# Performance work log

Measured on AMD Instinct MI355X. Metric: run time of the kernel, lower is better.

Reference implementation:

```python
import jax, jax.numpy as jnp
import numpy as np


def setup_inputs() -> dict:
    key = jax.random.key(0)
    ks = jax.random.split(key, 3)
    B, H, W, C = 32, 56, 56, 512
    N = H * W
    x = jax.random.normal(ks[0], (B, N, C), dtype=jnp.float32)
    # learned params (qkv_bias=False)
    w_qkv = jax.random.normal(ks[1], (C, 3 * C), dtype=jnp.float32) * (C ** -0.5)
    w_proj = jax.random.normal(ks[2], (C, C), dtype=jnp.float32) * (C ** -0.5)
    b_proj = jnp.zeros((C,), dtype=jnp.float32)
    return {"x": x, "w_qkv": w_qkv, "w_proj": w_proj, "b_proj": b_proj,
            "H": H, "W": W}


def reference(x, w_qkv, w_proj, b_proj, H, W):
    num_heads, ws = 8, 7
    B, N, C = x.shape
    hd = C // num_heads
    scale = hd ** -0.5
    hg, wg = H // ws, W // ws
    G = hg * wg  # total groups
    S = ws * ws  # tokens per window
    # window partition: [B,N,C] -> [B,G,S,C]
    xw = x.reshape(B, hg, ws, wg, ws, C).transpose(0, 1, 3, 2, 4, 5)
    xw = xw.reshape(B, G, S, C)
    # qkv projection -> [3,B,G,heads,S,hd]
    qkv = (xw @ w_qkv).reshape(B, G, S, 3, num_heads, hd)
    qkv = qkv.transpose(3, 0, 1, 4, 2, 5)
    q, k, v = qkv[0], qkv[1], qkv[2]
    attn = jnp.einsum('bghqd,bghkd->bghqk', q, k) * scale
    attn = jax.nn.softmax(attn, axis=-1)
    out = jnp.einsum('bghqk,bghkd->bghqd', attn, v)
    # merge heads: [B,G,h,S,d] -> [B,G,S,C]
    out = out.transpose(0, 1, 3, 2, 4).reshape(B, G, S, C)
    # window merge: [B,G,S,C] -> [B,N,C]
    out = out.reshape(B, hg, wg, ws, ws, C).transpose(0, 1, 3, 2, 4, 5)
    out = out.reshape(B, N, C)
    return out @ w_proj + b_proj
```

## Files before the change

### kernel.cpp

```cpp
#include <hip/hip_runtime.h>

typedef unsigned short ushort;
typedef unsigned int uint;
typedef __bf16 bf16x8 __attribute__((ext_vector_type(8)));
typedef unsigned short u16x8 __attribute__((ext_vector_type(8)));
typedef float f32x4 __attribute__((ext_vector_type(4)));

__device__ __forceinline__ ushort f2bf(float f) {
  uint u = __builtin_bit_cast(uint, f);
  u += 0x7fffu + ((u >> 16) & 1u);
  return (ushort)(u >> 16);
}

__device__ __forceinline__ f32x4 mfma_bf16(u16x8 a, u16x8 b, f32x4 c) {
  return __builtin_amdgcn_mfma_f32_16x16x32_bf16(
      __builtin_bit_cast(bf16x8, a), __builtin_bit_cast(bf16x8, b), c, 0, 0, 0);
}

__global__ __launch_bounds__(256) void cvt_x(const float* __restrict__ X,
                                             ushort* __restrict__ Xb, int total8) {
  int stride = gridDim.x * 256;
  for (int i = blockIdx.x * 256 + threadIdx.x; i < total8; i += stride) {
    f32x4 a = ((const f32x4*)X)[2 * i];
    f32x4 b = ((const f32x4*)X)[2 * i + 1];
    u16x8 o;
#pragma unroll
    for (int j = 0; j < 4; ++j) { o[j] = f2bf(a[j]); o[j + 4] = f2bf(b[j]); }
    ((u16x8*)Xb)[i] = o;
  }
}

__global__ __launch_bounds__(256) void transpose_cvt(const float* __restrict__ W,
                                                     ushort* __restrict__ WT,
                                                     int K, int N) {
  __shared__ float t[32][33];
  const int tn0 = blockIdx.x * 32, tk0 = blockIdx.y * 32;
  const int tx = threadIdx.x & 31, ty = threadIdx.x >> 5;
#pragma unroll
  for (int i = 0; i < 4; ++i) {
    int k = tk0 + ty + i * 8;
    t[ty + i * 8][tx] = W[(size_t)k * N + tn0 + tx];
  }
  __syncthreads();
#pragma unroll
  for (int i = 0; i < 4; ++i) {
    int n = tn0 + ty + i * 8;
    WT[(size_t)n * K + tk0 + tx] = f2bf(t[tx][ty + i * 8]);
  }
}


#define GLL(g, l)                                                              \
  __builtin_amdgcn_global_load_lds(                                            \
      (const __attribute__((address_space(1))) uint*)(g),                      \
      (__attribute__((address_space(3))) uint*)(l), 16, 0, 0)
#define BAR() __builtin_amdgcn_s_barrier()
#define SCB() __builtin_amdgcn_sched_barrier(0)
#define WAITV(n) asm volatile("s_waitcnt vmcnt(" #n ")" ::: "memory")

template <int OUT>
__global__ __launch_bounds__(512, 2) void gemm8p(const ushort* __restrict__ A,
                                                 const ushort* __restrict__ BT,
                                                 void* __restrict__ Cout,
                                                 const float* __restrict__ bias,
                                                 const int ldc, const int NT,
                                                 const int CPX) {
  __shared__ __align__(16) ushort as_[2][16384];
  __shared__ __align__(16) ushort bs_[2][16384];
  const int bid = blockIdx.x;
  const int wg = (bid & 7) * CPX + (bid >> 3);
  const int mt = wg / NT, nt = wg - mt * NT;
  const int m0 = mt << 8, n0 = nt << 8;
  const int tid = threadIdx.x, lane = tid & 63, wid = tid >> 6;
  const int wm = wid >> 2, wn = wid & 3;
  const int c16 = lane & 15, q4 = lane >> 4;
  const int sw = c16 & 7;
  const int lrow = lane >> 3, lcg = (lane & 7) ^ lrow;
  const ushort* Ag = A + (size_t)(m0 + wid * 16 + lrow) * 512 + lcg * 8;
  const ushort* Bg = BT + (size_t)(n0 + wid * 16 + lrow) * 512 + lcg * 8;
  const int aro = (wm * 64 + c16) * 64;
  const int bro = (wn * 32 + c16) * 64;
  const int ag0 = (q4 ^ sw) * 8;
  const int ag1 = ((4 + q4) ^ sw) * 8;

  f32x4 acc[8][4];
#pragma unroll
  for (int m = 0; m < 8; ++m)
#pragma unroll
    for (int n = 0; n < 4; ++n) acc[m][n] = f32x4{0.f, 0.f, 0.f, 0.f};
  u16x8 af[4][2], bf0[2][2], bf1[2][2];

#define STAGE_A(half, ktg)                                                     \
  do {                                                                         \
    const ushort* g_ = Ag + (size_t)(half) * (128 * 512) + (ktg) * 64;         \
    ushort* l_ = &as_[(ktg) & 1][(half) * 8192 + wid * 1024 + lane * 8];       \
    GLL(g_, l_);                                                               \
    GLL(g_ + 8 * 512, l_ + 512);                                               \
  } while (0)
#define STAGE_B(half, ktg)                                                     \
  do {                                                                         \
    const ushort* g_ = Bg + (size_t)(half) * (128 * 512) + (ktg) * 64;         \
    ushort* l_ = &bs_[(ktg) & 1][(half) * 8192 + wid * 1024 + lane * 8];       \
    GLL(g_, l_);                                                               \
    GLL(g_ + 8 * 512, l_ + 512);                                               \
  } while (0)
#define LDA(kt, mh)                                                            \
  do {                                                                         \
    const ushort* p_ = &as_[kt][(mh)*8192 + aro];                              \
    _Pragma("unroll") for (int f_ = 0; f_ < 4; ++f_) {                         \
      af[f_][0] = *(const u16x8*)(p_ + f_ * 1024 + ag0);                       \
      af[f_][1] = *(const u16x8*)(p_ + f_ * 1024 + ag1);                       \
    }                                                                          \
  } while (0)
#define LDB(kt, nh, BF)                                                        \
  do {                                                                         \
    const ushort* p_ = &bs_[kt][(nh)*8192 + bro];                              \
    _Pragma("unroll") for (int g_ = 0; g_ < 2; ++g_) {                         \
      BF[g_][0] = *(const u16x8*)(p_ + g_ * 1024 + ag0);                       \
      BF[g_][1] = *(const u16x8*)(p_ + g_ * 1024 + ag1);                       \
    }                                                                          \
  } while (0)
#define MM(mh, nh, BF)                                                         \
  do {                                                                         \
    __builtin_amdgcn_s_setprio(1);                                             \
    _Pragma("unroll") for (int f_ = 0; f_ < 4; ++f_)                           \
        _Pragma("unroll") for (int g_ = 0; g_ < 2; ++g_) {                     \
      f32x4& a_ = acc[(mh)*4 + f_][(nh)*2 + g_];                               \
      a_ = mfma_bf16(af[f_][0], BF[g_][0], a_);                                \
      a_ = mfma_bf16(af[f_][1], BF[g_][1], a_);                                \
    }                                                                          \
    __builtin_amdgcn_s_setprio(0);                                             \
  } while (0)

  STAGE_A(0, 0); STAGE_B(1, 0); STAGE_B(0, 0);
  STAGE_A(1, 0); STAGE_A(0, 1); STAGE_B(1, 1);
  WAITV(6); BAR(); SCB();

  for (int i = 0; i < 3; ++i) {
    const int k1g = 2 * i + 1, k2g = 2 * i + 2, k3g = 2 * i + 3;
    LDA(0, 0); LDB(0, 0, bf0); STAGE_A(1, k1g);
    BAR(); MM(0, 0, bf0); WAITV(10); BAR(); SCB();
    LDB(0, 1, bf1); STAGE_B(0, k1g);
    BAR(); MM(0, 1, bf1); WAITV(8); BAR(); SCB();
    LDA(0, 1); STAGE_A(0, k2g);
    BAR(); MM(1, 1, bf1); BAR(); SCB();
    STAGE_B(1, k2g);
    BAR(); MM(1, 0, bf0); WAITV(4); BAR(); SCB();
    LDA(1, 0); LDB(1, 0, bf0); STAGE_B(0, k2g);
    BAR(); MM(0, 0, bf0); WAITV(10); BAR(); SCB();
    LDB(1, 1, bf1); STAGE_A(1, k2g);
    BAR(); MM(0, 1, bf1); WAITV(10); BAR(); SCB();
    LDA(1, 1); STAGE_A(0, k3g);
    BAR(); MM(1, 1, bf1); BAR(); SCB();
    STAGE_B(1, k3g);
    BAR(); MM(1, 0, bf0); WAITV(6); BAR(); SCB();
  }
  {
    LDA(0, 0); LDB(0, 0, bf0); STAGE_A(1, 7);
    BAR(); MM(0, 0, bf0); WAITV(10); BAR(); SCB();
    LDB(0, 1, bf1); STAGE_B(0, 7);
    BAR(); MM(0, 1, bf1); WAITV(8); BAR(); SCB();
    LDA(0, 1);
    BAR(); MM(1, 1, bf1); BAR(); SCB();
    BAR(); MM(1, 0, bf0); WAITV(0); BAR(); SCB();
    LDA(1, 0); LDB(1, 0, bf0);
    BAR(); MM(0, 0, bf0); BAR(); SCB();
    LDB(1, 1, bf1);
    BAR(); MM(0, 1, bf1); BAR(); SCB();
    LDA(1, 1);
    BAR(); MM(1, 1, bf1); BAR(); SCB();
    BAR(); MM(1, 0, bf0);
  }

  const int crow = m0 + wm * 64 + q4 * 4;
  const int ccol = n0 + wn * 32 + c16;
  if constexpr (OUT == 0) {
    ushort* C = (ushort*)Cout;
#pragma unroll
    for (int mf = 0; mf < 8; ++mf) {
      const int ro = (mf >> 2) * 128 + (mf & 3) * 16;
#pragma unroll
      for (int r = 0; r < 4; ++r) {
        ushort* cp = C + (size_t)(crow + ro + r) * ldc + ccol;
        cp[0]   = f2bf(acc[mf][0][r]);
        cp[16]  = f2bf(acc[mf][1][r]);
        cp[128] = f2bf(acc[mf][2][r]);
        cp[144] = f2bf(acc[mf][3][r]);
      }
    }
  } else {
    float* C = (float*)Cout;
    const float b0 = bias[ccol], b1 = bias[ccol + 16];
    const float b2 = bias[ccol + 128], b3 = bias[ccol + 144];
#pragma unroll
    for (int mf = 0; mf < 8; ++mf) {
      const int ro = (mf >> 2) * 128 + (mf & 3) * 16;
#pragma unroll
      for (int r = 0; r < 4; ++r) {
        float* cp = C + (size_t)(crow + ro + r) * ldc + ccol;
        cp[0]   = acc[mf][0][r] + b0;
        cp[16]  = acc[mf][1][r] + b1;
        cp[128] = acc[mf][2][r] + b2;
        cp[144] = acc[mf][3][r] + b3;
      }
    }
  }
#undef STAGE_A
#undef STAGE_B
#undef LDA
#undef LDB
#undef MM
}

__global__ __launch_bounds__(256) void attn_win(const ushort* __restrict__ qkv,
                                                ushort* __restrict__ O) {
  __shared__ __align__(16) ushort p_lds[4][4096];
  __shared__ __align__(16) ushort v_lds[4][4096];
  const int tid = threadIdx.x, lane = tid & 63, w = tid >> 6;
  const int wg = blockIdx.x * 4 + w;
  const int head = wg & 7, g = (wg >> 3) & 63, b = wg >> 9;
  const int gh = g >> 3, gw = g & 7;
  const int c16 = lane & 15, q4 = lane >> 4;
  const size_t brow = (size_t)b * 3136;
  const u16x8 Z = {0, 0, 0, 0, 0, 0, 0, 0};

  int rowq[4]; bool val[4];
#pragma unroll
  for (int i = 0; i < 4; ++i) {
    int s = i * 16 + c16;
    val[i] = (s < 49);
    int ss = val[i] ? s : 0;
    rowq[i] = (gh * 7 + ss / 7) * 56 + gw * 7 + ss % 7;
  }
  const int qc = head * 64 + q4 * 8;

  u16x8 qf[2][4], kf[2][4];
#pragma unroll
  for (int i = 0; i < 4; ++i) {
    const ushort* p = qkv + (brow + rowq[i]) * 1536 + qc;
#pragma unroll
    for (int kk = 0; kk < 2; ++kk) {
      qf[kk][i] = val[i] ? *reinterpret_cast<const u16x8*>(p + kk * 32) : Z;
      kf[kk][i] = val[i] ? *reinterpret_cast<const u16x8*>(p + 512 + kk * 32) : Z;
    }
  }

  {
    int t = lane < 49 ? lane : 0;
    const ushort* vp =
        qkv + (brow + ((gh * 7 + t / 7) * 56 + gw * 7 + t % 7)) * 1536 + 1024 + head * 64;
    u16x8 vr[8];
#pragma unroll
    for (int j = 0; j < 8; ++j)
      vr[j] = (lane < 49) ? *reinterpret_cast<const u16x8*>(vp + j * 8) : Z;
#pragma unroll
    for (int d = 0; d < 64; ++d)
      v_lds[w][(d * 64 + lane) ^ ((d & 7) << 3)] = vr[d >> 3][d & 7];
  }

  f32x4 acc[4][4];
#pragma unroll
  for (int m = 0; m < 4; ++m)
#pragma unroll
    for (int n = 0; n < 4; ++n) acc[m][n] = f32x4{0.f, 0.f, 0.f, 0.f};
#pragma unroll
  for (int kk = 0; kk < 2; ++kk)
#pragma unroll
    for (int m = 0; m < 4; ++m)
#pragma unroll
      for (int n = 0; n < 4; ++n)
        acc[m][n] = mfma_bf16(qf[kk][m], kf[kk][n], acc[m][n]);

#pragma unroll
  for (int m = 0; m < 4; ++m)
#pragma unroll
    for (int r = 0; r < 4; ++r) {
      float s0 = acc[m][0][r] * 0.125f;
      float s1 = acc[m][1][r] * 0.125f;
      float s2 = acc[m][2][r] * 0.125f;
      float s3 = (c16 == 0) ? acc[m][3][r] * 0.125f : -1e30f;
      float mx = fmaxf(fmaxf(s0, s1), fmaxf(s2, s3));
#pragma unroll
      for (int off = 1; off < 16; off <<= 1) mx = fmaxf(mx, __shfl_xor(mx, off));
      s0 = __expf(s0 - mx);
      s1 = __expf(s1 - mx);
      s2 = __expf(s2 - mx);
      s3 = (c16 == 0) ? __expf(s3 - mx) : 0.f;
      float sum = s0 + s1 + s2 + s3;
#pragma unroll
      for (int off = 1; off < 16; off <<= 1) sum += __shfl_xor(sum, off);
      float inv = 1.f / sum;
      int row = m * 16 + q4 * 4 + r;
      int rb = row * 64, sw = (row & 7) << 3;
      p_lds[w][(rb + c16) ^ sw]      = f2bf(s0 * inv);
      p_lds[w][(rb + 16 + c16) ^ sw] = f2bf(s1 * inv);
      p_lds[w][(rb + 32 + c16) ^ sw] = f2bf(s2 * inv);
      p_lds[w][(rb + 48 + c16) ^ sw] = f2bf(s3 * inv);
    }
  __syncthreads();

  f32x4 o[4][4];
#pragma unroll
  for (int m = 0; m < 4; ++m)
#pragma unroll
    for (int n = 0; n < 4; ++n) o[m][n] = f32x4{0.f, 0.f, 0.f, 0.f};
#pragma unroll
  for (int kk = 0; kk < 2; ++kk) {
    u16x8 pa[4], vb[4];
#pragma unroll
    for (int m = 0; m < 4; ++m) {
      int row = m * 16 + c16;
      pa[m] = *reinterpret_cast<const u16x8*>(
          &p_lds[w][(row * 64 + kk * 32 + q4 * 8) ^ ((row & 7) << 3)]);
    }
#pragma unroll
    for (int n = 0; n < 4; ++n) {
      int d = n * 16 + c16;
      vb[n] = *reinterpret_cast<const u16x8*>(
          &v_lds[w][(d * 64 + kk * 32 + q4 * 8) ^ ((d & 7) << 3)]);
    }
#pragma unroll
    for (int m = 0; m < 4; ++m)
#pragma unroll
      for (int n = 0; n < 4; ++n) o[m][n] = mfma_bf16(pa[m], vb[n], o[m][n]);
  }

#pragma unroll
  for (int m = 0; m < 4; ++m)
#pragma unroll
    for (int r = 0; r < 4; ++r) {
      int s = m * 16 + q4 * 4 + r;
      if (s < 49) {
        int n_tok = (gh * 7 + s / 7) * 56 + gw * 7 + s % 7;
        ushort* op = O + (brow + n_tok) * 512 + head * 64 + c16;
        op[0]  = f2bf(o[m][0][r]);
        op[16] = f2bf(o[m][1][r]);
        op[32] = f2bf(o[m][2][r]);
        op[48] = f2bf(o[m][3][r]);
      }
    }
}

extern "C" void kernel_launch(void* const* d_in, const int* in_sizes, int n_in,
                              void* d_out, int out_size, void* d_ws, size_t ws_size,
                              hipStream_t stream) {
  const float* x      = (const float*)d_in[0];
  const float* w_qkv  = (const float*)d_in[1];
  const float* w_proj = (const float*)d_in[2];
  const float* b_proj = (const float*)d_in[3];
  char* ws = (char*)d_ws;
  ushort* wqkvT  = (ushort*)ws;
  ushort* wprojT = (ushort*)(ws + 1572864);
  ushort* xb     = (ushort*)(ws + 2097152);
  ushort* qkv    = (ushort*)(ws + 104857600);
  float* out = (float*)d_out;

  transpose_cvt<<<dim3(48, 16), 256, 0, stream>>>(w_qkv, wqkvT, 512, 1536);
  transpose_cvt<<<dim3(16, 16), 256, 0, stream>>>(w_proj, wprojT, 512, 512);
  cvt_x<<<2048, 256, 0, stream>>>(x, xb, 100352 * 512 / 8);
  gemm8p<0><<<2352, 512, 0, stream>>>(xb, wqkvT, (void*)qkv, nullptr, 1536, 6, 294);
  attn_win<<<4096, 256, 0, stream>>>(qkv, xb);
  gemm8p<1><<<784, 512, 0, stream>>>(xb, wprojT, (void*)out, b_proj, 512, 2, 98);
}
```

Before: 488.5 us.

## Reorder tokens into window-major layout and rework GEMM prefetch schedule

The input conversion kernel now gathers rows into window-major order, so the QKV GEMM output and the attention kernel see each 7x7 window as 49 contiguous rows. The output projection scatters rows back to the original token order in its epilogue. This replaces scattered per-token gathers in attention with contiguous row access. The GEMM main loop's stage/wait ordering is also reshuffled, with a deeper initial prefetch and different vmcnt waits, which may change how well loads overlap with MFMA work.

```diff
diff --git a/kernel.cpp b/kernel.cpp
--- a/kernel.cpp
+++ b/kernel.cpp
@@ -17,12 +17,20 @@
       __builtin_bit_cast(bf16x8, a), __builtin_bit_cast(bf16x8, b), c, 0, 0, 0);
 }
 
-__global__ __launch_bounds__(256) void cvt_x(const float* __restrict__ X,
-                                             ushort* __restrict__ Xb, int total8) {
+__device__ __forceinline__ uint win2orig(uint wr) {
+  uint b = wr / 3136u, rem = wr % 3136u;
+  uint g = rem / 49u, s = rem % 49u;
+  return b * 3136u + ((g >> 3) * 7u + s / 7u) * 56u + (g & 7u) * 7u + s % 7u;
+}
+
+__global__ __launch_bounds__(256) void cvt_x_win(const float* __restrict__ X,
+                                                 ushort* __restrict__ Xb, int total8) {
   int stride = gridDim.x * 256;
   for (int i = blockIdx.x * 256 + threadIdx.x; i < total8; i += stride) {
-    f32x4 a = ((const f32x4*)X)[2 * i];
-    f32x4 b = ((const f32x4*)X)[2 * i + 1];
+    uint wr = (uint)i >> 6, c8 = (uint)i & 63u;
+    const float* xp = X + (size_t)win2orig(wr) * 512 + c8 * 8;
+    f32x4 a = *(const f32x4*)xp;
+    f32x4 b = *(const f32x4*)(xp + 4);
     u16x8 o;
 #pragma unroll
     for (int j = 0; j < 4; ++j) { o[j] = f2bf(a[j]); o[j + 4] = f2bf(b[j]); }
@@ -132,45 +140,43 @@
     __builtin_amdgcn_s_setprio(0);                                             \
   } while (0)
 
-  STAGE_A(0, 0); STAGE_B(1, 0); STAGE_B(0, 0);
-  STAGE_A(1, 0); STAGE_A(0, 1); STAGE_B(1, 1);
-  WAITV(6); BAR(); SCB();
+  STAGE_A(0, 0); STAGE_B(0, 0); STAGE_B(1, 0); STAGE_A(1, 0);
+  STAGE_A(0, 1); STAGE_B(0, 1); STAGE_B(1, 1);
+  WAITV(10); BAR(); SCB();
 
   for (int i = 0; i < 3; ++i) {
-    const int k1g = 2 * i + 1, k2g = 2 * i + 2, k3g = 2 * i + 3;
-    LDA(0, 0); LDB(0, 0, bf0); STAGE_A(1, k1g);
+    const int o1 = 2 * i + 1, e2 = 2 * i + 2, o3 = 2 * i + 3;
+    LDA(0, 0); LDB(0, 0, bf0); STAGE_A(1, o1);
     BAR(); MM(0, 0, bf0); WAITV(10); BAR(); SCB();
-    LDB(0, 1, bf1); STAGE_B(0, k1g);
-    BAR(); MM(0, 1, bf1); WAITV(8); BAR(); SCB();
-    LDA(0, 1); STAGE_A(0, k2g);
+    LDB(0, 1, bf1); STAGE_A(0, e2);
+    BAR(); MM(0, 1, bf1); WAITV(10); BAR(); SCB();
+    LDA(0, 1); STAGE_B(0, e2);
     BAR(); MM(1, 1, bf1); BAR(); SCB();
-    STAGE_B(1, k2g);
-    BAR(); MM(1, 0, bf0); WAITV(4); BAR(); SCB();
-    LDA(1, 0); LDB(1, 0, bf0); STAGE_B(0, k2g);
+    STAGE_B(1, e2);
+    BAR(); MM(1, 0, bf0); WAITV(10); BAR(); SCB();
+    LDA(1, 0); LDB(1, 0, bf0); STAGE_A(1, e2);
     BAR(); MM(0, 0, bf0); WAITV(10); BAR(); SCB();
-    LDB(1, 1, bf1); STAGE_A(1, k2g);
+    LDB(1, 1, bf1); STAGE_A(0, o3);
     BAR(); MM(0, 1, bf1); WAITV(10); BAR(); SCB();
-    LDA(1, 1); STAGE_A(0, k3g);
+    LDA(1, 1); STAGE_B(0, o3);
     BAR(); MM(1, 1, bf1); BAR(); SCB();
-    STAGE_B(1, k3g);
-    BAR(); MM(1, 0, bf0); WAITV(6); BAR(); SCB();
-  }
-  {
-    LDA(0, 0); LDB(0, 0, bf0); STAGE_A(1, 7);
-    BAR(); MM(0, 0, bf0); WAITV(10); BAR(); SCB();
-    LDB(0, 1, bf1); STAGE_B(0, 7);
-    BAR(); MM(0, 1, bf1); WAITV(8); BAR(); SCB();
-    LDA(0, 1);
-    BAR(); MM(1, 1, bf1); BAR(); SCB();
-    BAR(); MM(1, 0, bf0); WAITV(0); BAR(); SCB();
-    LDA(1, 0); LDB(1, 0, bf0);
-    BAR(); MM(0, 0, bf0); BAR(); SCB();
-    LDB(1, 1, bf1);
-    BAR(); MM(0, 1, bf1); BAR(); SCB();
-    LDA(1, 1);
-    BAR(); MM(1, 1, bf1); BAR(); SCB();
-    BAR(); MM(1, 0, bf0);
-  }
+    STAGE_B(1, o3);
+    BAR(); MM(1, 0, bf0); WAITV(10); BAR(); SCB();
+  }
+  LDA(0, 0); LDB(0, 0, bf0); STAGE_A(1, 7);
+  BAR(); MM(0, 0, bf0); WAITV(10); BAR(); SCB();
+  LDB(0, 1, bf1);
+  BAR(); MM(0, 1, bf1); WAITV(8); BAR(); SCB();
+  LDA(0, 1);
+  BAR(); MM(1, 1, bf1); BAR(); SCB();
+  BAR(); MM(1, 0, bf0); WAITV(4); BAR(); SCB();
+  LDA(1, 0); LDB(1, 0, bf0);
+  BAR(); MM(0, 0, bf0); WAITV(2); BAR(); SCB();
+  LDB(1, 1, bf1);
+  BAR(); MM(0, 1, bf1); WAITV(0); BAR(); SCB();
+  LDA(1, 1);
+  BAR(); MM(1, 1, bf1); BAR(); SCB();
+  BAR(); MM(1, 0, bf0);
 
   const int crow = m0 + wm * 64 + q4 * 4;
   const int ccol = n0 + wn * 32 + c16;
@@ -197,7 +203,7 @@
       const int ro = (mf >> 2) * 128 + (mf & 3) * 16;
 #pragma unroll
       for (int r = 0; r < 4; ++r) {
-        float* cp = C + (size_t)(crow + ro + r) * ldc + ccol;
+        float* cp = C + (size_t)win2orig((uint)(crow + ro + r)) * 512 + ccol;
         cp[0]   = acc[mf][0][r] + b0;
         cp[16]  = acc[mf][1][r] + b1;
         cp[128] = acc[mf][2][r] + b2;
@@ -219,36 +225,26 @@
   const int tid = threadIdx.x, lane = tid & 63, w = tid >> 6;
   const int wg = blockIdx.x * 4 + w;
   const int head = wg & 7, g = (wg >> 3) & 63, b = wg >> 9;
-  const int gh = g >> 3, gw = g & 7;
   const int c16 = lane & 15, q4 = lane >> 4;
-  const size_t brow = (size_t)b * 3136;
+  const size_t wrow = (size_t)b * 3136 + g * 49;
   const u16x8 Z = {0, 0, 0, 0, 0, 0, 0, 0};
 
-  int rowq[4]; bool val[4];
+  const int qc = head * 64 + q4 * 8;
+  u16x8 qf[2][4], kf[2][4];
 #pragma unroll
   for (int i = 0; i < 4; ++i) {
     int s = i * 16 + c16;
-    val[i] = (s < 49);
-    int ss = val[i] ? s : 0;
-    rowq[i] = (gh * 7 + ss / 7) * 56 + gw * 7 + ss % 7;
-  }
-  const int qc = head * 64 + q4 * 8;
-
-  u16x8 qf[2][4], kf[2][4];
-#pragma unroll
-  for (int i = 0; i < 4; ++i) {
-    const ushort* p = qkv + (brow + rowq[i]) * 1536 + qc;
+    bool val = (s < 49);
+    const ushort* p = qkv + (wrow + (val ? s : 0)) * 1536 + qc;
 #pragma unroll
     for (int kk = 0; kk < 2; ++kk) {
-      qf[kk][i] = val[i] ? *reinterpret_cast<const u16x8*>(p + kk * 32) : Z;
-      kf[kk][i] = val[i] ? *reinterpret_cast<const u16x8*>(p + 512 + kk * 32) : Z;
+      qf[kk][i] = val ? *reinterpret_cast<const u16x8*>(p + kk * 32) : Z;
+      kf[kk][i] = val ? *reinterpret_cast<const u16x8*>(p + 512 + kk * 32) : Z;
     }
   }
 
   {
-    int t = lane < 49 ? lane : 0;
-    const ushort* vp =
-        qkv + (brow + ((gh * 7 + t / 7) * 56 + gw * 7 + t % 7)) * 1536 + 1024 + head * 64;
+    const ushort* vp = qkv + (wrow + (lane < 49 ? lane : 0)) * 1536 + 1024 + head * 64;
     u16x8 vr[8];
 #pragma unroll
     for (int j = 0; j < 8; ++j)
@@ -291,11 +287,11 @@
       for (int off = 1; off < 16; off <<= 1) sum += __shfl_xor(sum, off);
       float inv = 1.f / sum;
       int row = m * 16 + q4 * 4 + r;
-      int rb = row * 64, sw = (row & 7) << 3;
-      p_lds[w][(rb + c16) ^ sw]      = f2bf(s0 * inv);
-      p_lds[w][(rb + 16 + c16) ^ sw] = f2bf(s1 * inv);
-      p_lds[w][(rb + 32 + c16) ^ sw] = f2bf(s2 * inv);
-      p_lds[w][(rb + 48 + c16) ^ sw] = f2bf(s3 * inv);
+      int rb = row * 64, swz = (row & 7) << 3;
+      p_lds[w][(rb + c16) ^ swz]      = f2bf(s0 * inv);
+      p_lds[w][(rb + 16 + c16) ^ swz] = f2bf(s1 * inv);
+      p_lds[w][(rb + 32 + c16) ^ swz] = f2bf(s2 * inv);
+      p_lds[w][(rb + 48 + c16) ^ swz] = f2bf(s3 * inv);
     }
   __syncthreads();
 
@@ -331,8 +327,7 @@
     for (int r = 0; r < 4; ++r) {
       int s = m * 16 + q4 * 4 + r;
       if (s < 49) {
-        int n_tok = (gh * 7 + s / 7) * 56 + gw * 7 + s % 7;
-        ushort* op = O + (brow + n_tok) * 512 + head * 64 + c16;
+        ushort* op = O + (wrow + s) * 512 + head * 64 + c16;
         op[0]  = f2bf(o[m][0][r]);
         op[16] = f2bf(o[m][1][r]);
         op[32] = f2bf(o[m][2][r]);
@@ -357,7 +352,7 @@
 
   transpose_cvt<<<dim3(48, 16), 256, 0, stream>>>(w_qkv, wqkvT, 512, 1536);
   transpose_cvt<<<dim3(16, 16), 256, 0, stream>>>(w_proj, wprojT, 512, 512);
-  cvt_x<<<2048, 256, 0, stream>>>(x, xb, 100352 * 512 / 8);
+  cvt_x_win<<<2048, 256, 0, stream>>>(x, xb, 100352 * 512 / 8);
   gemm8p<0><<<2352, 512, 0, stream>>>(xb, wqkvT, (void*)qkv, nullptr, 1536, 6, 294);
   attn_win<<<4096, 256, 0, stream>>>(qkv, xb);
   gemm8p<1><<<784, 512, 0, stream>>>(xb, wprojT, (void*)out, b_proj, 512, 2, 98);
```

Measured after the change: 491.2 us. About the same (+0.6%).
